# Kernel optimization log

Measured on AMD Instinct MI355X. Metric: run time of the kernel, lower is better.

The kernel has to match this reference:

```python
import jax, jax.numpy as jnp
import numpy as np

RADIUS = 12
SIGMA = 5.0
T0 = 0.1
TOP_PERCENT = 0.1
CURVE_STEPS = 8


def _gaussian_kernel():
    xs = jnp.arange(-RADIUS, RADIUS + 1, dtype=jnp.float32)
    k = jnp.exp(-0.5 * jnp.square(xs / SIGMA))
    k = k / jnp.sum(k)
    k2 = k[:, None] * k[None, :]
    # depthwise kernel (O=3, I/group=1, 25, 25)
    return jnp.tile(k2[None, None], (3, 1, 1, 1))


def tanh01(x):
    return (jnp.tanh(x) + 1) / 2


def tanh_range(l, r):
    return lambda x: tanh01(x) * (r - l) + l


def _parse_params(p):
    omega = tanh_range(0.1, 1.0)(p[:, 0:1])                          # (B,1)
    wb_mask = jnp.array([0.0, 1.0, 1.0], dtype=p.dtype)[None]
    wb = jnp.exp(tanh_range(-0.5, 0.5)(p[:, 1:4] * wb_mask))         # (B,3)
    lg = jnp.log(jnp.asarray(3.0, dtype=p.dtype))
    gamma = jnp.exp(tanh_range(-lg, lg)(p[:, 4:5]))                  # (B,1)
    tone = tanh_range(0.5, 2.0)(p[:, 5:13].reshape(-1, 1, 8)[:, None, None, :])  # (B,1,1,1,8)
    contrast = jnp.tanh(p[:, 13:14])                                 # (B,1)
    sharpen = tanh_range(0.0, 5.0)(p[:, 14:15])                      # (B,1)
    return omega, wb, gamma, tone, contrast, sharpen


def _apply_defog(x, omega):
    # mirror `if x.min() < 0: x = (x+1)/2` in a jit-safe way
    x = jnp.where(jnp.min(x) < 0, (x + 1) / 2, x)
    B, C, H, W = x.shape
    dark = jnp.min(x, axis=1)                                        # (B,H,W)
    k = int(H * W * TOP_PERCENT)
    flat = dark.reshape(B, H * W)
    _, idx = jax.lax.top_k(flat, k)                                  # (B,k)
    xf = x.reshape(B, C, H * W)
    sel = jnp.take_along_axis(xf, idx[:, None, :], axis=2)           # (B,C,k)
    A = jnp.max(sel, axis=2)[:, :, None, None]                       # (B,C,1,1)
    t = jnp.clip(1 - omega[:, :, None] * dark, T0, 1.0)[:, None]     # (B,1,H,W)
    J = (x - A) / t + A
    return jnp.clip(J, 0.0, 1.0)


def _apply_white_balance(image, wb):
    denom = (0.27 * wb[:, 0] + 0.67 * wb[:, 1] + 0.06 * wb[:, 2] + 1e-05)[:, None]
    p = wb / denom
    return image * p[:, :, None, None]


def _apply_gamma(image, gamma):
    g = jnp.tile(gamma, (1, 3))[:, :, None, None]                    # (B,3,1,1)
    return jnp.power(jnp.maximum(image, 1e-4), g)


def _apply_tone(image, tone):
    tone_sum = jnp.sum(tone, axis=-1) + 1e-30                        # (B,1,1,1)
    total = jnp.zeros_like(image)
    for i in range(CURVE_STEPS):
        total = total + jnp.clip(image - 1.0 * i / CURVE_STEPS, 0.0, 1.0 / CURVE_STEPS) * tone[:, :, :, :, i]
    return total * CURVE_STEPS / tone_sum


def _apply_contrast(image, contrast):
    # faithful to source: rgb2lum indexes the LAST axis (W), giving (B,3,H,1)
    lum = (0.27 * image[:, :, :, 0] + 0.67 * image[:, :, :, 1] + 0.06 * image[:, :, :, 2])[:, :, :, None]
    lum = jnp.clip(lum, 0.0, 1.0)
    contrast_lum = -jnp.cos(jnp.pi * lum) * 0.5 + 0.5
    contrast_image = image / (lum + 1e-6) * contrast_lum
    c = contrast[:, :, None, None]                                   # (B,1,1,1)
    return (1 - c) * image + c * contrast_image


def _apply_sharpen(image, sharpen):
    kernel = _gaussian_kernel()
    blurred = jax.lax.conv_general_dilated(
        image, kernel, window_strides=(1, 1),
        padding=[(RADIUS, RADIUS), (RADIUS, RADIUS)],
        dimension_numbers=('NCHW', 'OIHW', 'NCHW'),
        feature_group_count=3)
    s = sharpen[:, None, None, :]                                    # (B,1,1,1)
    return (image - blurred) * s + image


def setup_inputs() -> dict:
    key = jax.random.key(0)
    k1, k2 = jax.random.split(key)
    x = jax.random.uniform(k1, (16, 3, 512, 512), dtype=jnp.float32)
    params = jax.random.normal(k2, (16, 15), dtype=jnp.float32)
    return {"x": x, "params": params}


def reference(x, params):
    omega, wb, gamma, tone, contrast, sharpen = _parse_params(params)
    image = _apply_defog(x, omega)
    image = _apply_white_balance(image, wb)
    image = _apply_gamma(image, gamma)
    image = _apply_tone(image, tone)
    image = _apply_contrast(image, contrast)
    image = _apply_sharpen(image, sharpen)
    return jax.nn.sigmoid(image)
```

## Files before the change

kernel.cpp:

```cpp
#include <hip/hip_runtime.h>
#include <math.h>

#define NB 16
#define NC 3
#define NH 512
#define NW 512
#define NHW (NH*NW)
#define KSEL 26214u
#define PI_F 3.14159265358979f
#define LOG2E_F 1.44269504f

typedef _Float16 half4v __attribute__((ext_vector_type(4)));
typedef _Float16 half8v __attribute__((ext_vector_type(8)));
typedef float    float4v __attribute__((ext_vector_type(4)));

#define TMPH_OFF   0
#define PCH_OFF    (NB*NC*NHW/2)
#define HIST_OFF   (PCH_OFF + NB*NC*NHW/2)
#define BMAX_OFF   (HIST_OFF + NB*256)
#define AVAL_OFF   (BMAX_OFF + NB*768)
#define PBUF_OFF   (AVAL_OFF + NB*3)
#define GW_OFF     (PBUF_OFF + NB*32)

__device__ __forceinline__ float fast_rcp(float x)  { return __builtin_amdgcn_rcpf(x); }
__device__ __forceinline__ float fast_exp2(float x) { return __builtin_amdgcn_exp2f(x); }
__device__ __forceinline__ float fast_log2(float x) { return __builtin_amdgcn_logf(x); }

__device__ __forceinline__ float chain_tt(float xv, float dv, float omega, float Aval,
                                          float wbp, float g, const float* tone) {
  float t = fminf(fmaxf(1.f - omega*dv, 0.1f), 1.f);
  float J = (xv - Aval)*fast_rcp(t) + Aval;
  J = fminf(fmaxf(J, 0.f), 1.f);
  float v = J * wbp;
  float u = fast_exp2(g * fast_log2(fmaxf(v, 1e-4f)));
  float tt = 0.f;
#pragma unroll
  for (int i = 0; i < 8; i++)
    tt = fmaf(fminf(fmaxf(u - 0.125f*(float)i, 0.f), 0.125f), tone[i], tt);
  return tt;
}

__global__ void k_params(const float* __restrict__ p, float* __restrict__ pbuf,
                         float* __restrict__ gw, unsigned* __restrict__ hist,
                         unsigned* __restrict__ binmax) {
  int b = blockIdx.x, tid = threadIdx.x;
  if (tid == 0) {
    const float* pp = p + b*15;
    float* ob = pbuf + b*32;
    float omega = (tanhf(pp[0])+1.f)*0.5f*0.9f + 0.1f;
    float wb0 = 1.0f;
    float wb1 = expf((tanhf(pp[2])+1.f)*0.5f - 0.5f);
    float wb2 = expf((tanhf(pp[3])+1.f)*0.5f - 0.5f);
    float denom = 0.27f*wb0 + 0.67f*wb1 + 0.06f*wb2 + 1e-5f;
    float lg = logf(3.0f);
    float g = expf((tanhf(pp[4])+1.f)*0.5f*(2.f*lg) - lg);
    float ts = 0.f, tone[8];
    for (int i = 0; i < 8; i++) { tone[i] = (tanhf(pp[5+i])+1.f)*0.5f*1.5f + 0.5f; ts += tone[i]; }
    ts += 1e-30f;
    ob[0] = omega; ob[1] = wb0/denom; ob[2] = wb1/denom; ob[3] = wb2/denom; ob[4] = g;
    for (int i = 0; i < 8; i++) ob[5+i] = tone[i];
    ob[13] = 8.0f/ts;
    ob[14] = tanhf(pp[13]);
    ob[15] = (tanhf(pp[14])+1.f)*0.5f*5.0f;
  }
  if (b == 0 && tid == 64) {
    float wv[25], wsum = 0.f;
    for (int i = 0; i < 25; i++) { float d = (float)(i-12)/5.0f; wv[i] = expf(-0.5f*d*d); wsum += wv[i]; }
    for (int i = 0; i < 25; i++) gw[i] = wv[i]/wsum;
  }
  hist[b*256 + tid] = 0u;
  for (int i = tid; i < 768; i += 256) binmax[b*768 + i] = 0u;
}

__global__ __launch_bounds__(256) void k_stats(const float* __restrict__ x,
                                               unsigned* __restrict__ hist,
                                               unsigned* __restrict__ binmax) {
  __shared__ unsigned lh[8*256];
  __shared__ unsigned lbm[4][768];
  int tid = threadIdx.x, b = blockIdx.y;
  for (int i = tid; i < 8*256; i += 256) lh[i] = 0u;
  for (int i = tid; i < 4*768; i += 256) ((unsigned*)lbm)[i] = 0u;
  __syncthreads();
  const float4* x0 = (const float4*)(x + (size_t)b*NC*NHW);
  const float4* x1 = x0 + NHW/4;
  const float4* x2 = x1 + NHW/4;
  unsigned* lhm = lh + (tid & 7)*256;
  unsigned* bmr = lbm[tid & 3];
  int base = blockIdx.x*1024 + tid;
#pragma unroll
  for (int it = 0; it < 4; it++) {
    int i = base + it*256;
    float4 a = x0[i], g = x1[i], r = x2[i];
    float dv[4] = { fminf(fminf(a.x,g.x),r.x), fminf(fminf(a.y,g.y),r.y),
                    fminf(fminf(a.z,g.z),r.z), fminf(fminf(a.w,g.w),r.w) };
    float av[4] = {a.x,a.y,a.z,a.w}, gv[4] = {g.x,g.y,g.z,g.w}, rv[4] = {r.x,r.y,r.z,r.w};
#pragma unroll
    for (int q = 0; q < 4; q++) {
      unsigned bin = __float_as_uint(dv[q]) >> 24;
      atomicAdd(&lhm[bin], 1u);
      atomicMax(&bmr[bin],       __float_as_uint(av[q]));
      atomicMax(&bmr[256 + bin], __float_as_uint(gv[q]));
      atomicMax(&bmr[512 + bin], __float_as_uint(rv[q]));
    }
  }
  __syncthreads();
  {
    unsigned s = 0;
    for (int r2 = 0; r2 < 8; r2++) s += lh[r2*256 + tid];
    if (s) atomicAdd(&hist[b*256 + tid], s);
  }
  for (int idx = tid; idx < 768; idx += 256) {
    unsigned m = lbm[0][idx];
    m = max(m, lbm[1][idx]); m = max(m, lbm[2][idx]); m = max(m, lbm[3][idx]);
    if (m) atomicMax(&binmax[b*768 + idx], m);
  }
}

__global__ void k_scan(const unsigned* __restrict__ hist,
                       const unsigned* __restrict__ binmax,
                       float* __restrict__ avals) {
  int b = blockIdx.x, lane = threadIdx.x;
  unsigned cnt[4], s = 0;
#pragma unroll
  for (int j = 0; j < 4; j++) { cnt[j] = hist[b*256 + (255 - (lane*4+j))]; s += cnt[j]; }
  unsigned inc = s;
  for (int off = 1; off < 64; off <<= 1) {
    unsigned n = __shfl_up(inc, off);
    if (lane >= off) inc += n;
  }
  unsigned excl = inc - s;
  bool found = (excl < KSEL && KSEL <= inc);
  int localBin = 0;
  if (found) {
    unsigned run = excl; int binj = 0;
#pragma unroll
    for (int j = 0; j < 4; j++) {
      unsigned nb = run + cnt[j];
      if (KSEL > run && KSEL <= nb) binj = j;
      run = nb;
    }
    localBin = 255 - (lane*4 + binj);
  }
  unsigned long long mask = __ballot(found ? 1 : 0);
  int src = (int)__ffsll((long long)mask) - 1;
  int bstar = __shfl(localBin, src);
#pragma unroll
  for (int c = 0; c < 3; c++) {
    float m = 0.f;
#pragma unroll
    for (int j = 0; j < 4; j++) {
      int bin = 255 - (lane*4 + j);
      if (bin >= bstar) m = fmaxf(m, __uint_as_float(binmax[b*768 + c*256 + bin]));
    }
    for (int off = 1; off < 64; off <<= 1) m = fmaxf(m, __shfl_xor(m, off));
    if (lane == 0) avals[b*3 + c] = m;
  }
}

__global__ __launch_bounds__(256) void k_hblur(
    const float* __restrict__ x, const float* __restrict__ pbuf,
    const float* __restrict__ avals, const float* __restrict__ gw,
    _Float16* __restrict__ tmph, _Float16* __restrict__ pch) {
  __shared__ __align__(16) float pcp[3][4][544];
  __shared__ float rfs[4][3];
  int tid = threadIdx.x;
  int row = tid >> 6, lane = tid & 63;
  int b = blockIdx.y;
  int h = blockIdx.x*4 + row;
  const float* pb = pbuf + b*32;
  float omega = pb[0], g = pb[4], ts = pb[13], cc = pb[14];
  float wbp[3] = {pb[1], pb[2], pb[3]};
  float tone[8];
#pragma unroll
  for (int i = 0; i < 8; i++) tone[i] = pb[5+i];
  float Av[3] = {avals[b*3], avals[b*3+1], avals[b*3+2]};
  if (lane < 16) {
#pragma unroll
    for (int c = 0; c < 3; c++) { pcp[c][row][lane] = 0.f; pcp[c][row][528 + lane] = 0.f; }
  }
  const float4* xr0 = (const float4*)(x + ((size_t)b*3 + 0)*NHW + (size_t)h*NW);
  const float4* xr1 = (const float4*)(x + ((size_t)b*3 + 1)*NHW + (size_t)h*NW);
  const float4* xr2 = (const float4*)(x + ((size_t)b*3 + 2)*NHW + (size_t)h*NW);
#pragma unroll
  for (int m = 0; m < 2; m++) {
    int i4 = lane + m*64;
    float4 v0 = xr0[i4], v1 = xr1[i4], v2 = xr2[i4];
    float4 d;
    d.x = fminf(fminf(v0.x,v1.x),v2.x); d.y = fminf(fminf(v0.y,v1.y),v2.y);
    d.z = fminf(fminf(v0.z,v1.z),v2.z); d.w = fminf(fminf(v0.w,v1.w),v2.w);
    float4 p0, p1, p2;
    p0.x = chain_tt(v0.x, d.x, omega, Av[0], wbp[0], g, tone);
    p0.y = chain_tt(v0.y, d.y, omega, Av[0], wbp[0], g, tone);
    p0.z = chain_tt(v0.z, d.z, omega, Av[0], wbp[0], g, tone);
    p0.w = chain_tt(v0.w, d.w, omega, Av[0], wbp[0], g, tone);
    p1.x = chain_tt(v1.x, d.x, omega, Av[1], wbp[1], g, tone);
    p1.y = chain_tt(v1.y, d.y, omega, Av[1], wbp[1], g, tone);
    p1.z = chain_tt(v1.z, d.z, omega, Av[1], wbp[1], g, tone);
    p1.w = chain_tt(v1.w, d.w, omega, Av[1], wbp[1], g, tone);
    p2.x = chain_tt(v2.x, d.x, omega, Av[2], wbp[2], g, tone);
    p2.y = chain_tt(v2.y, d.y, omega, Av[2], wbp[2], g, tone);
    p2.z = chain_tt(v2.z, d.z, omega, Av[2], wbp[2], g, tone);
    p2.w = chain_tt(v2.w, d.w, omega, Av[2], wbp[2], g, tone);
    *(float4*)&pcp[0][row][16 + i4*4] = p0;
    *(float4*)&pcp[1][row][16 + i4*4] = p1;
    *(float4*)&pcp[2][row][16 + i4*4] = p2;
  }
  __syncthreads();
  if (lane < 3) {
    int c = lane;
    float p0 = pcp[c][row][16]*ts, p1 = pcp[c][row][17]*ts, p2 = pcp[c][row][18]*ts;
    float lum = fminf(fmaxf(0.27f*p0 + 0.67f*p1 + 0.06f*p2, 0.f), 1.f);
    float cl = 0.5f - 0.5f*__cosf(PI_F*lum);
    rfs[row][c] = ts*((1.f - cc) + cc*cl*fast_rcp(lum + 1e-6f));
  }
  __syncthreads();
  float kw[25];
#pragma unroll
  for (int j = 0; j < 25; j++) kw[j] = gw[j];
#pragma unroll
  for (int c = 0; c < 3; c++) {
    float rfv = rfs[row][c];
    float acc[8] = {0,0,0,0,0,0,0,0};
    const float* rowp = &pcp[c][row][lane*8 + 4];
#pragma unroll
    for (int r = 0; r < 8; r++) {
      float4 v = *(const float4*)(rowp + r*4);
      float vs[4] = {v.x, v.y, v.z, v.w};
#pragma unroll
      for (int q = 0; q < 4; q++) {
        int idx = r*4 + q;
#pragma unroll
        for (int i = 0; i < 8; i++) {
          int j = idx - i;
          if (j >= 0 && j < 25) acc[i] = fmaf(kw[j], vs[q], acc[i]);
        }
      }
    }
    size_t off = ((size_t)b*3 + c)*NHW + (size_t)h*NW + lane*8;
    half8v th;
#pragma unroll
    for (int i = 0; i < 8; i++) th[i] = (_Float16)(acc[i]*rfv);
    *(half8v*)(tmph + off) = th;
    float4 c0 = *(float4*)&pcp[c][row][16 + lane*8];
    float4 c1 = *(float4*)&pcp[c][row][20 + lane*8];
    half8v ph;
    ph[0] = (_Float16)(c0.x*rfv); ph[1] = (_Float16)(c0.y*rfv);
    ph[2] = (_Float16)(c0.z*rfv); ph[3] = (_Float16)(c0.w*rfv);
    ph[4] = (_Float16)(c1.x*rfv); ph[5] = (_Float16)(c1.y*rfv);
    ph[6] = (_Float16)(c1.z*rfv); ph[7] = (_Float16)(c1.w*rfv);
    *(half8v*)(pch + off) = ph;
  }
}

__global__ __launch_bounds__(256) void k_vblur(
    const _Float16* __restrict__ tmph, const _Float16* __restrict__ pch,
    const float* __restrict__ pbuf, const float* __restrict__ gw,
    float* __restrict__ out) {
  __shared__ _Float16 sh[152*64];
  int tid = threadIdx.x;
  int bc = blockIdx.z, b = bc/3;
  int w0 = blockIdx.x*64, h0 = blockIdx.y*128;
  const _Float16* tr = tmph + (size_t)bc*NHW;
  for (int idx = tid; idx < 152*8; idx += 256) {
    int r = idx >> 3, seg = idx & 7;
    int gh = h0 - 12 + r;
    uint4 v = make_uint4(0u,0u,0u,0u);
    if (gh >= 0 && gh < NH) v = *(const uint4*)(tr + (size_t)gh*NW + w0 + seg*8);
    *(uint4*)&sh[r*64 + seg*8] = v;
  }
  __syncthreads();
  float kw[25];
#pragma unroll
  for (int j = 0; j < 25; j++) kw[j] = gw[j];
  int wq = tid & 15, rg = tid >> 4;
  int rowbase = rg*8;
  float4v acc[8];
#pragma unroll
  for (int i = 0; i < 8; i++) acc[i] = (float4v)0.f;
#pragma unroll
  for (int r = 0; r < 32; r++) {
    half4v hv = *(const half4v*)&sh[(rowbase + r)*64 + wq*4];
    float4v v = __builtin_convertvector(hv, float4v);
#pragma unroll
    for (int i = 0; i < 8; i++) {
      int j = r - i;
      if (j >= 0 && j < 25) acc[i] += kw[j]*v;
    }
  }
  float sharp = pbuf[b*32 + 15];
#pragma unroll
  for (int i = 0; i < 8; i++) {
    int h = h0 + rowbase + i;
    size_t off = (size_t)bc*NHW + (size_t)h*NW + w0 + wq*4;
    half4v pcv = *(const half4v*)(pch + off);
    float4v pc = __builtin_convertvector(pcv, float4v);
    float4v res = (pc - acc[i])*sharp + pc;
    float4v o;
    o.x = fast_rcp(1.f + fast_exp2(-res.x*LOG2E_F));
    o.y = fast_rcp(1.f + fast_exp2(-res.y*LOG2E_F));
    o.z = fast_rcp(1.f + fast_exp2(-res.z*LOG2E_F));
    o.w = fast_rcp(1.f + fast_exp2(-res.w*LOG2E_F));
    *(float4v*)(out + off) = o;
  }
}

extern "C" void kernel_launch(void* const* d_in, const int* in_sizes, int n_in,
                              void* d_out, int out_size, void* d_ws, size_t ws_size,
                              hipStream_t stream) {
  const float* x = (const float*)d_in[0];
  const float* params = (const float*)d_in[1];
  float* out = (float*)d_out;
  float* ws = (float*)d_ws;

  _Float16* tmph = (_Float16*)(ws + TMPH_OFF);
  _Float16* pch  = (_Float16*)(ws + PCH_OFF);
  unsigned* hist   = (unsigned*)(ws + HIST_OFF);
  unsigned* binmax = (unsigned*)(ws + BMAX_OFF);
  float* avals = ws + AVAL_OFF;
  float* pbuf  = ws + PBUF_OFF;
  float* gw    = ws + GW_OFF;

  k_params<<<NB, 256, 0, stream>>>(params, pbuf, gw, hist, binmax);
  k_stats<<<dim3(64, NB), 256, 0, stream>>>(x, hist, binmax);
  k_scan<<<NB, 64, 0, stream>>>(hist, binmax, avals);
  k_hblur<<<dim3(NH/4, NB), 256, 0, stream>>>(x, pbuf, avals, gw, tmph, pch);
  k_vblur<<<dim3(NW/64, NH/128, NB*NC), 256, 0, stream>>>(tmph, pch, pbuf, gw, out);
}
```

Baseline: 151.5 us.

## Fuse horizontal and vertical blur into one tiled kernel with halo recompute

Replaces the separate horizontal-blur and vertical-blur kernels, which round-tripped fp16 intermediates through global memory, with a single 2D-tiled kernel. Each block loads a 128x64 tile plus a 12-pixel halo from x, recomputes the pointwise chain and the per-row contrast factor in shared memory, then runs both blur passes and the sigmoid in place. This removes the intermediate global writes and reads. In exchange it recomputes the expensive per-pixel chain on halo pixels and reloads all three input channels once per output channel.

```diff
diff --git a/kernel.cpp b/kernel.cpp
--- a/kernel.cpp
+++ b/kernel.cpp
@@ -10,14 +10,18 @@
 #define PI_F 3.14159265358979f
 #define LOG2E_F 1.44269504f
 
+#define TW 128
+#define TH 64
+#define RAD 12
+#define PCW (TW + 2*RAD)
+#define PRH (TH + 2*RAD)
+
 typedef _Float16 half4v __attribute__((ext_vector_type(4)));
 typedef _Float16 half8v __attribute__((ext_vector_type(8)));
 typedef float    float4v __attribute__((ext_vector_type(4)));
 
-#define TMPH_OFF   0
-#define PCH_OFF    (NB*NC*NHW/2)
-#define HIST_OFF   (PCH_OFF + NB*NC*NHW/2)
-#define BMAX_OFF   (HIST_OFF + NB*256)
+#define HIST_OFF   0
+#define BMAX_OFF   (NB*256)
 #define AVAL_OFF   (BMAX_OFF + NB*768)
 #define PBUF_OFF   (AVAL_OFF + NB*3)
 #define GW_OFF     (PBUF_OFF + NB*32)
@@ -157,150 +161,134 @@
   }
 }
 
-__global__ __launch_bounds__(256) void k_hblur(
+__global__ __launch_bounds__(512) void k_conv(
     const float* __restrict__ x, const float* __restrict__ pbuf,
     const float* __restrict__ avals, const float* __restrict__ gw,
-    _Float16* __restrict__ tmph, _Float16* __restrict__ pch) {
-  __shared__ __align__(16) float pcp[3][4][544];
-  __shared__ float rfs[4][3];
+    float* __restrict__ out) {
+  __shared__ _Float16 s_pc[PRH*PCW];
+  __shared__ _Float16 s_hb[PRH*TW];
+  __shared__ float s_rf[3][PRH];
   int tid = threadIdx.x;
-  int row = tid >> 6, lane = tid & 63;
-  int b = blockIdx.y;
-  int h = blockIdx.x*4 + row;
+  int b = blockIdx.z;
+  int w0 = blockIdx.x*TW, h0 = blockIdx.y*TH;
   const float* pb = pbuf + b*32;
-  float omega = pb[0], g = pb[4], ts = pb[13], cc = pb[14];
+  float omega = pb[0], g = pb[4], ts = pb[13], cc = pb[14], sharp = pb[15];
   float wbp[3] = {pb[1], pb[2], pb[3]};
   float tone[8];
 #pragma unroll
   for (int i = 0; i < 8; i++) tone[i] = pb[5+i];
   float Av[3] = {avals[b*3], avals[b*3+1], avals[b*3+2]};
-  if (lane < 16) {
-#pragma unroll
-    for (int c = 0; c < 3; c++) { pcp[c][row][lane] = 0.f; pcp[c][row][528 + lane] = 0.f; }
-  }
-  const float4* xr0 = (const float4*)(x + ((size_t)b*3 + 0)*NHW + (size_t)h*NW);
-  const float4* xr1 = (const float4*)(x + ((size_t)b*3 + 1)*NHW + (size_t)h*NW);
-  const float4* xr2 = (const float4*)(x + ((size_t)b*3 + 2)*NHW + (size_t)h*NW);
-#pragma unroll
-  for (int m = 0; m < 2; m++) {
-    int i4 = lane + m*64;
-    float4 v0 = xr0[i4], v1 = xr1[i4], v2 = xr2[i4];
-    float4 d;
-    d.x = fminf(fminf(v0.x,v1.x),v2.x); d.y = fminf(fminf(v0.y,v1.y),v2.y);
-    d.z = fminf(fminf(v0.z,v1.z),v2.z); d.w = fminf(fminf(v0.w,v1.w),v2.w);
-    float4 p0, p1, p2;
-    p0.x = chain_tt(v0.x, d.x, omega, Av[0], wbp[0], g, tone);
-    p0.y = chain_tt(v0.y, d.y, omega, Av[0], wbp[0], g, tone);
-    p0.z = chain_tt(v0.z, d.z, omega, Av[0], wbp[0], g, tone);
-    p0.w = chain_tt(v0.w, d.w, omega, Av[0], wbp[0], g, tone);
-    p1.x = chain_tt(v1.x, d.x, omega, Av[1], wbp[1], g, tone);
-    p1.y = chain_tt(v1.y, d.y, omega, Av[1], wbp[1], g, tone);
-    p1.z = chain_tt(v1.z, d.z, omega, Av[1], wbp[1], g, tone);
-    p1.w = chain_tt(v1.w, d.w, omega, Av[1], wbp[1], g, tone);
-    p2.x = chain_tt(v2.x, d.x, omega, Av[2], wbp[2], g, tone);
-    p2.y = chain_tt(v2.y, d.y, omega, Av[2], wbp[2], g, tone);
-    p2.z = chain_tt(v2.z, d.z, omega, Av[2], wbp[2], g, tone);
-    p2.w = chain_tt(v2.w, d.w, omega, Av[2], wbp[2], g, tone);
-    *(float4*)&pcp[0][row][16 + i4*4] = p0;
-    *(float4*)&pcp[1][row][16 + i4*4] = p1;
-    *(float4*)&pcp[2][row][16 + i4*4] = p2;
-  }
-  __syncthreads();
-  if (lane < 3) {
-    int c = lane;
-    float p0 = pcp[c][row][16]*ts, p1 = pcp[c][row][17]*ts, p2 = pcp[c][row][18]*ts;
-    float lum = fminf(fmaxf(0.27f*p0 + 0.67f*p1 + 0.06f*p2, 0.f), 1.f);
-    float cl = 0.5f - 0.5f*__cosf(PI_F*lum);
-    rfs[row][c] = ts*((1.f - cc) + cc*cl*fast_rcp(lum + 1e-6f));
-  }
-  __syncthreads();
   float kw[25];
 #pragma unroll
   for (int j = 0; j < 25; j++) kw[j] = gw[j];
+  const float* xb = x + (size_t)b*3*NHW;
+
+  if (tid < PRH) {
+    int gh = h0 - RAD + tid;
+    if (gh >= 0 && gh < NH) {
+      float xv[3][3], dk[3];
+#pragma unroll
+      for (int c = 0; c < 3; c++)
+#pragma unroll
+        for (int w = 0; w < 3; w++) xv[c][w] = xb[(size_t)c*NHW + (size_t)gh*NW + w];
+#pragma unroll
+      for (int w = 0; w < 3; w++) dk[w] = fminf(fminf(xv[0][w],xv[1][w]),xv[2][w]);
+#pragma unroll
+      for (int c = 0; c < 3; c++) {
+        float p0 = chain_tt(xv[c][0], dk[0], omega, Av[c], wbp[c], g, tone)*ts;
+        float p1 = chain_tt(xv[c][1], dk[1], omega, Av[c], wbp[c], g, tone)*ts;
+        float p2 = chain_tt(xv[c][2], dk[2], omega, Av[c], wbp[c], g, tone)*ts;
+        float lum = fminf(fmaxf(0.27f*p0 + 0.67f*p1 + 0.06f*p2, 0.f), 1.f);
+        float cl = 0.5f - 0.5f*__cosf(PI_F*lum);
+        s_rf[c][tid] = ts*((1.f - cc) + cc*cl*fast_rcp(lum + 1e-6f));
+      }
+    } else {
+      s_rf[0][tid] = 0.f; s_rf[1][tid] = 0.f; s_rf[2][tid] = 0.f;
+    }
+  }
+
 #pragma unroll
   for (int c = 0; c < 3; c++) {
-    float rfv = rfs[row][c];
-    float acc[8] = {0,0,0,0,0,0,0,0};
-    const float* rowp = &pcp[c][row][lane*8 + 4];
-#pragma unroll
-    for (int r = 0; r < 8; r++) {
-      float4 v = *(const float4*)(rowp + r*4);
-      float vs[4] = {v.x, v.y, v.z, v.w};
-#pragma unroll
-      for (int q = 0; q < 4; q++) {
-        int idx = r*4 + q;
-#pragma unroll
-        for (int i = 0; i < 8; i++) {
-          int j = idx - i;
-          if (j >= 0 && j < 25) acc[i] = fmaf(kw[j], vs[q], acc[i]);
+    __syncthreads();
+    for (int idx = tid; idx < PRH*(PCW/4); idx += 512) {
+      int r = idx / (PCW/4);
+      int q = idx - r*(PCW/4);
+      int gh = h0 - RAD + r;
+      int gwc = w0 - RAD + q*4;
+      bool in = (gh >= 0) && (gh < NH) && (gwc >= 0) && (gwc < NW);
+      float4 v0 = make_float4(0.f,0.f,0.f,0.f), v1 = v0, v2 = v0;
+      if (in) {
+        size_t base = (size_t)gh*NW + gwc;
+        v0 = *(const float4*)(xb + base);
+        v1 = *(const float4*)(xb + NHW + base);
+        v2 = *(const float4*)(xb + 2*(size_t)NHW + base);
+      }
+      float rfv = in ? s_rf[c][r] : 0.f;
+      float4 vc = (c == 0) ? v0 : ((c == 1) ? v1 : v2);
+      float d0 = fminf(fminf(v0.x,v1.x),v2.x);
+      float d1 = fminf(fminf(v0.y,v1.y),v2.y);
+      float d2 = fminf(fminf(v0.z,v1.z),v2.z);
+      float d3 = fminf(fminf(v0.w,v1.w),v2.w);
+      half4v hv;
+      hv[0] = (_Float16)(chain_tt(vc.x, d0, omega, Av[c], wbp[c], g, tone)*rfv);
+      hv[1] = (_Float16)(chain_tt(vc.y, d1, omega, Av[c], wbp[c], g, tone)*rfv);
+      hv[2] = (_Float16)(chain_tt(vc.z, d2, omega, Av[c], wbp[c], g, tone)*rfv);
+      hv[3] = (_Float16)(chain_tt(vc.w, d3, omega, Av[c], wbp[c], g, tone)*rfv);
+      *(half4v*)&s_pc[r*PCW + q*4] = hv;
+    }
+    __syncthreads();
+    for (int idx = tid; idx < PRH*(TW/8); idx += 512) {
+      int r = idx >> 4, gq = idx & 15;
+      const _Float16* rp = &s_pc[r*PCW + gq*8];
+      half8v a0 = *(const half8v*)rp;
+      half8v a1 = *(const half8v*)(rp + 8);
+      half8v a2 = *(const half8v*)(rp + 16);
+      half8v a3 = *(const half8v*)(rp + 24);
+      float v[32];
+#pragma unroll
+      for (int k2 = 0; k2 < 8; k2++) {
+        v[k2]      = (float)a0[k2]; v[8+k2]  = (float)a1[k2];
+        v[16+k2]   = (float)a2[k2]; v[24+k2] = (float)a3[k2];
+      }
+      float acc[8] = {0,0,0,0,0,0,0,0};
+#pragma unroll
+      for (int i = 0; i < 8; i++)
+#pragma unroll
+        for (int j = 0; j < 25; j++) acc[i] = fmaf(kw[j], v[i+j], acc[i]);
+      half8v o;
+#pragma unroll
+      for (int k2 = 0; k2 < 8; k2++) o[k2] = (_Float16)acc[k2];
+      *(half8v*)&s_hb[r*TW + gq*8] = o;
+    }
+    __syncthreads();
+    {
+      int wq = tid & 31, rg = tid >> 5;
+      int rbase = rg*4;
+      float4v acc[4] = {(float4v)0.f, (float4v)0.f, (float4v)0.f, (float4v)0.f};
+#pragma unroll
+      for (int j = 0; j < 28; j++) {
+        half4v hv = *(const half4v*)&s_hb[(rbase + j)*TW + wq*4];
+        float4v v = __builtin_convertvector(hv, float4v);
+#pragma unroll
+        for (int i = 0; i < 4; i++) {
+          int k2 = j - i;
+          if (k2 >= 0 && k2 < 25) acc[i] += kw[k2]*v;
         }
       }
-    }
-    size_t off = ((size_t)b*3 + c)*NHW + (size_t)h*NW + lane*8;
-    half8v th;
-#pragma unroll
-    for (int i = 0; i < 8; i++) th[i] = (_Float16)(acc[i]*rfv);
-    *(half8v*)(tmph + off) = th;
-    float4 c0 = *(float4*)&pcp[c][row][16 + lane*8];
-    float4 c1 = *(float4*)&pcp[c][row][20 + lane*8];
-    half8v ph;
-    ph[0] = (_Float16)(c0.x*rfv); ph[1] = (_Float16)(c0.y*rfv);
-    ph[2] = (_Float16)(c0.z*rfv); ph[3] = (_Float16)(c0.w*rfv);
-    ph[4] = (_Float16)(c1.x*rfv); ph[5] = (_Float16)(c1.y*rfv);
-    ph[6] = (_Float16)(c1.z*rfv); ph[7] = (_Float16)(c1.w*rfv);
-    *(half8v*)(pch + off) = ph;
-  }
-}
-
-__global__ __launch_bounds__(256) void k_vblur(
-    const _Float16* __restrict__ tmph, const _Float16* __restrict__ pch,
-    const float* __restrict__ pbuf, const float* __restrict__ gw,
-    float* __restrict__ out) {
-  __shared__ _Float16 sh[152*64];
-  int tid = threadIdx.x;
-  int bc = blockIdx.z, b = bc/3;
-  int w0 = blockIdx.x*64, h0 = blockIdx.y*128;
-  const _Float16* tr = tmph + (size_t)bc*NHW;
-  for (int idx = tid; idx < 152*8; idx += 256) {
-    int r = idx >> 3, seg = idx & 7;
-    int gh = h0 - 12 + r;
-    uint4 v = make_uint4(0u,0u,0u,0u);
-    if (gh >= 0 && gh < NH) v = *(const uint4*)(tr + (size_t)gh*NW + w0 + seg*8);
-    *(uint4*)&sh[r*64 + seg*8] = v;
-  }
-  __syncthreads();
-  float kw[25];
-#pragma unroll
-  for (int j = 0; j < 25; j++) kw[j] = gw[j];
-  int wq = tid & 15, rg = tid >> 4;
-  int rowbase = rg*8;
-  float4v acc[8];
-#pragma unroll
-  for (int i = 0; i < 8; i++) acc[i] = (float4v)0.f;
-#pragma unroll
-  for (int r = 0; r < 32; r++) {
-    half4v hv = *(const half4v*)&sh[(rowbase + r)*64 + wq*4];
-    float4v v = __builtin_convertvector(hv, float4v);
-#pragma unroll
-    for (int i = 0; i < 8; i++) {
-      int j = r - i;
-      if (j >= 0 && j < 25) acc[i] += kw[j]*v;
-    }
-  }
-  float sharp = pbuf[b*32 + 15];
-#pragma unroll
-  for (int i = 0; i < 8; i++) {
-    int h = h0 + rowbase + i;
-    size_t off = (size_t)bc*NHW + (size_t)h*NW + w0 + wq*4;
-    half4v pcv = *(const half4v*)(pch + off);
-    float4v pc = __builtin_convertvector(pcv, float4v);
-    float4v res = (pc - acc[i])*sharp + pc;
-    float4v o;
-    o.x = fast_rcp(1.f + fast_exp2(-res.x*LOG2E_F));
-    o.y = fast_rcp(1.f + fast_exp2(-res.y*LOG2E_F));
-    o.z = fast_rcp(1.f + fast_exp2(-res.z*LOG2E_F));
-    o.w = fast_rcp(1.f + fast_exp2(-res.w*LOG2E_F));
-    *(float4v*)(out + off) = o;
+#pragma unroll
+      for (int i = 0; i < 4; i++) {
+        int r = rbase + i;
+        half4v pcv = *(const half4v*)&s_pc[(r + RAD)*PCW + RAD + wq*4];
+        float4v pcf = __builtin_convertvector(pcv, float4v);
+        float4v res = (pcf - acc[i])*sharp + pcf;
+        float4v o;
+        o.x = fast_rcp(1.f + fast_exp2(-res.x*LOG2E_F));
+        o.y = fast_rcp(1.f + fast_exp2(-res.y*LOG2E_F));
+        o.z = fast_rcp(1.f + fast_exp2(-res.z*LOG2E_F));
+        o.w = fast_rcp(1.f + fast_exp2(-res.w*LOG2E_F));
+        *(float4v*)(out + ((size_t)b*3 + c)*NHW + (size_t)(h0 + r)*NW + w0 + wq*4) = o;
+      }
+    }
   }
 }
 
@@ -312,8 +300,6 @@
   float* out = (float*)d_out;
   float* ws = (float*)d_ws;
 
-  _Float16* tmph = (_Float16*)(ws + TMPH_OFF);
-  _Float16* pch  = (_Float16*)(ws + PCH_OFF);
   unsigned* hist   = (unsigned*)(ws + HIST_OFF);
   unsigned* binmax = (unsigned*)(ws + BMAX_OFF);
   float* avals = ws + AVAL_OFF;
@@ -323,6 +309,5 @@
   k_params<<<NB, 256, 0, stream>>>(params, pbuf, gw, hist, binmax);
   k_stats<<<dim3(64, NB), 256, 0, stream>>>(x, hist, binmax);
   k_scan<<<NB, 64, 0, stream>>>(hist, binmax, avals);
-  k_hblur<<<dim3(NH/4, NB), 256, 0, stream>>>(x, pbuf, avals, gw, tmph, pch);
-  k_vblur<<<dim3(NW/64, NH/128, NB*NC), 256, 0, stream>>>(tmph, pch, pbuf, gw, out);
-}
+  k_conv<<<dim3(NW/TW, NH/TH, NB), 512, 0, stream>>>(x, pbuf, avals, gw, out);
+}
```

New measurement: 175.0 us. +15.5%, slower.
